# Kernel tuning notes

Measured on AMD Instinct MI355X. Metric: run time of the kernel, lower is better.

The kernel has to match this reference:

```python
import jax, jax.numpy as jnp
import numpy as np

# Representation: lvals=[0,1] -> nreps NL=2, dim DIM=1+3=4; mult=8; kqv conv out_mult=3*mult
N, K, EDGE_DIM, HID = 10000, 16, 32, 64
MULT, NL, DIM = 8, 2, 4
OUT_MULT = 3 * MULT
E = N * K
NHEADS = 4
HEAD_DIM = MULT * DIM // NHEADS  # 8


def setup_inputs() -> dict:
    key = jax.random.key(0)
    ks = jax.random.split(key, 9)
    out_flat = NL * NL * MULT * OUT_MULT  # 768
    return {
        "basis1": jax.random.normal(ks[0], (E, DIM, NL), jnp.float32),
        "basis2": jax.random.normal(ks[1], (E, NL, DIM), jnp.float32),
        "edge_feats": jax.random.normal(ks[2], (E, EDGE_DIM), jnp.float32),
        "f": jax.random.normal(ks[3], (N, MULT, DIM), jnp.float32),
        "W1": jax.random.normal(ks[4], (HID, EDGE_DIM), jnp.float32) / np.sqrt(EDGE_DIM).astype(np.float32),
        "b1": jnp.zeros((HID,), jnp.float32),
        "W2": jax.random.normal(ks[5], (out_flat, HID), jnp.float32) / np.sqrt(HID).astype(np.float32),
        "b2": jnp.zeros((out_flat,), jnp.float32),
        "neighbor_idx": jax.random.randint(ks[6], (N, K), 0, N, dtype=jnp.int32),
    }


def reference(basis1, basis2, edge_feats, f, W1, b1, W2, b2, neighbor_idx):
    src = neighbor_idx.reshape(-1)  # (E,) source node per edge
    # RadialWeight: 2-layer MLP edge_feats -> per-edge TP weights (E, NL*OUT_MULT, NL*MULT)
    h = jax.nn.relu(edge_feats @ W1.T + b1)
    rw = (h @ W2.T + b2).reshape(E, NL * OUT_MULT, NL * MULT)
    # EquivariantConvolution: gather + small batched matmuls
    f_src = f[src]  # (E, MULT, DIM)
    tmp = jnp.einsum('emd,edl->eml', f_src, basis1).reshape(E, NL * MULT, 1)
    tmp = (rw @ tmp).reshape(E, OUT_MULT, NL)
    kqv = jnp.einsum('eml,eld->emd', tmp, basis2)  # (E, 3*MULT, DIM)
    # split fused k/q/v along multiplicity (repr_h.rep2.mult = 3*mult)
    k_, q_, v_ = jnp.split(kqv.reshape(N, K, OUT_MULT, DIM), 3, axis=2)  # each (N,K,MULT,DIM)
    k_ = k_.reshape(N, K, NHEADS, HEAD_DIM)
    v_ = v_.reshape(N, K, NHEADS, HEAD_DIM)
    q_node = q_.reshape(N, K, NHEADS, HEAD_DIM).mean(axis=1)  # per-node query (N,H,hd)
    scale = HEAD_DIM ** -0.5
    scores = jnp.einsum('nhd,nkhd->nhk', q_node, k_) * scale  # (N,H,K)
    w = jax.nn.softmax(scores, axis=-1)
    out = jnp.einsum('nhk,nkhd->nhd', w, v_)  # (N,H,hd)
    return out.reshape(N, MULT, DIM)
```

## Files before the change

kernel.cpp:

```cpp
#include <hip/hip_runtime.h>
#include <hip/hip_bf16.h>
#include <math.h>

#define N_NODES 10000
#define KNBR    16
#define EDGEF   32
#define HID     64
#define MULT    8
#define NL      2
#define DIM     4
#define OUT_MULT 24
#define NHEADS  4
#define HEAD_DIM 8
#define E_TOT   (N_NODES*KNBR)

#define EPB 128
#define TPB 128
#define NTILE 4
#define NODES_PB 8
#define NSLICE 33

typedef float    f32x4 __attribute__((ext_vector_type(4)));
typedef _Float16 f16x8 __attribute__((ext_vector_type(8)));

#define BF1_HALVES (4*64*8)
#define BF2_HALVES (3*NSLICE*64*8)
#define WS_HALVES  (BF1_HALVES + BF2_HALVES)

__global__ __launch_bounds__(256)
void esa_prep(const float* __restrict__ W1, const float* __restrict__ W2,
              const float* __restrict__ b2, _Float16* __restrict__ wsh)
{
    int i = blockIdx.x * 256 + threadIdx.x;
    if (i >= WS_HALVES) return;
    float v;
    if (i < BF1_HALVES) {
        int j = i & 7, lane = (i >> 3) & 63, t = i >> 9;
        int k = ((lane >> 4) << 3) + j;
        int n = (t << 4) + (lane & 15);
        v = W1[n * EDGEF + k];
    } else {
        int i2 = i - BF1_HALVES;
        int j = i2 & 7, lane = (i2 >> 3) & 63;
        int st = i2 >> 9;
        int s = st % NSLICE, t = st / NSLICE;
        int k = (s << 5) + ((lane >> 4) << 3) + j;
        int n = (t << 4) + (lane & 15);
        if (k < 1024)      v = W2[(n * 16 + (k >> 6)) * HID + (k & 63)];
        else if (k < 1040) v = b2[n * 16 + (k - 1024)];
        else               v = 0.f;
    }
    wsh[i] = (_Float16)v;
}

__global__ __launch_bounds__(TPB, 2)
void esa_main(const float* __restrict__ basis1, const float* __restrict__ basis2,
              const float* __restrict__ edge_feats, const float* __restrict__ f,
              const float* __restrict__ b1, const int* __restrict__ nbr,
              const _Float16* __restrict__ wsh, float* __restrict__ out)
{
    __shared__ __align__(16) unsigned char smem[32768];
    _Float16* hls = (_Float16*)smem;
    _Float16* tpl = (_Float16*)(smem + 18432);
    float*    t2  = (float*)smem;
    float*    b2l = (float*)(smem + 26624);

    const int tid  = threadIdx.x;
    const int eb   = blockIdx.x * EPB;
    const int lane = tid & 63;
    const int w    = tid >> 6;
    const int lo   = lane & 15, hi = lane >> 4;

    {
        const int el = tid;
        const int e  = eb + el;
        const int src = nbr[e];
        const float4* b1p = (const float4*)(basis1 + (size_t)e * 8);
        float4 u0 = b1p[0], u1 = b1p[1];
        float bl0[4] = {u0.x, u0.z, u1.x, u1.z};
        float bl1[4] = {u0.y, u0.w, u1.y, u1.w};
        const float4* fp = (const float4*)(f + (size_t)src * 32);
        _Float16 tpv[16];
        #pragma unroll
        for (int m = 0; m < 8; ++m) {
            float4 fv = fp[m];
            float a0 = fv.x*bl0[0] + fv.y*bl0[1] + fv.z*bl0[2] + fv.w*bl0[3];
            float a1 = fv.x*bl1[0] + fv.y*bl1[1] + fv.z*bl1[2] + fv.w*bl1[3];
            tpv[m*2+0] = (_Float16)a0;
            tpv[m*2+1] = (_Float16)a1;
        }
        *(f16x8*)(tpl + el*16)     = *(f16x8*)&tpv[0];
        *(f16x8*)(tpl + el*16 + 8) = *(f16x8*)&tpv[8];
        const float4* b2p = (const float4*)(basis2 + (size_t)e * 8);
        *(float4*)(b2l + el*12)     = b2p[0];
        *(float4*)(b2l + el*12 + 4) = b2p[1];
    }

    {
        float b1v[4];
        #pragma unroll
        for (int t = 0; t < 4; ++t) b1v[t] = b1[t*16 + lo];
        f16x8 afr[NTILE];
        #pragma unroll
        for (int mt = 0; mt < NTILE; ++mt) {
            size_t eg = (size_t)(eb + w*64 + mt*16 + lo);
            const float4* p = (const float4*)(edge_feats + eg*32 + hi*8);
            float4 x0 = p[0], x1 = p[1];
            f16x8 a;
            a[0]=(_Float16)x0.x; a[1]=(_Float16)x0.y; a[2]=(_Float16)x0.z; a[3]=(_Float16)x0.w;
            a[4]=(_Float16)x1.x; a[5]=(_Float16)x1.y; a[6]=(_Float16)x1.z; a[7]=(_Float16)x1.w;
            afr[mt] = a;
        }
        #pragma unroll
        for (int t = 0; t < 4; ++t) {
            f16x8 bfr = *(const f16x8*)(wsh + ((size_t)(t*64 + lane)) * 8);
            #pragma unroll
            for (int mt = 0; mt < NTILE; ++mt) {
                f32x4 acc = {0.f, 0.f, 0.f, 0.f};
                acc = __builtin_amdgcn_mfma_f32_16x16x32_f16(afr[mt], bfr, acc, 0, 0, 0);
                #pragma unroll
                for (int r = 0; r < 4; ++r) {
                    float hv = acc[r] + b1v[t];
                    hv = hv > 0.f ? hv : 0.f;
                    int el = w*64 + mt*16 + hi*4 + r;
                    hls[el*72 + t*16 + lo] = (_Float16)hv;
                }
            }
        }
    }
    __syncthreads();

    f32x4 acc[NTILE][3];
    #pragma unroll
    for (int mt = 0; mt < NTILE; ++mt)
        #pragma unroll
        for (int t = 0; t < 3; ++t)
            acc[mt][t] = (f32x4){0.f, 0.f, 0.f, 0.f};

    {
        const _Float16* Bf2 = wsh + BF1_HALVES;
        const _Float16* hp[NTILE];
        f16x8 tpA[NTILE], tpB[NTILE];
        #pragma unroll
        for (int mt = 0; mt < NTILE; ++mt) {
            const int e_mt = w*64 + mt*16 + lo;
            hp[mt]  = hls + e_mt*72 + hi*8;
            tpA[mt] = *(const f16x8*)(tpl + e_mt*16);
            tpB[mt] = *(const f16x8*)(tpl + e_mt*16 + 8);
        }

        #pragma unroll
        for (int s = 0; s < 32; ++s) {
            const int c  = s >> 1;
            const int sh = s & 1;
            f16x8 bfr[3];
            #pragma unroll
            for (int t = 0; t < 3; ++t)
                bfr[t] = *(const f16x8*)(Bf2 + ((size_t)((t*NSLICE + s)*64 + lane)) * 8);
            #pragma unroll
            for (int mt = 0; mt < NTILE; ++mt) {
                _Float16 t0 = (c < 8) ? tpA[mt][c & 7] : tpB[mt][c & 7];
                f16x8 ts = {t0,t0,t0,t0,t0,t0,t0,t0};
                f16x8 h  = *(const f16x8*)(hp[mt] + sh*32);
                f16x8 a  = h * ts;
                #pragma unroll
                for (int t = 0; t < 3; ++t)
                    acc[mt][t] = __builtin_amdgcn_mfma_f32_16x16x32_f16(a, bfr[t], acc[mt][t], 0, 0, 0);
            }
        }
        {
            f16x8 z = {(_Float16)0,(_Float16)0,(_Float16)0,(_Float16)0,
                       (_Float16)0,(_Float16)0,(_Float16)0,(_Float16)0};
            f16x8 bfr[3];
            #pragma unroll
            for (int t = 0; t < 3; ++t)
                bfr[t] = *(const f16x8*)(Bf2 + ((size_t)((t*NSLICE + 32)*64 + lane)) * 8);
            #pragma unroll
            for (int mt = 0; mt < NTILE; ++mt) {
                f16x8 a = (hi == 0) ? tpA[mt] : (hi == 1) ? tpB[mt] : z;
                #pragma unroll
                for (int t = 0; t < 3; ++t)
                    acc[mt][t] = __builtin_amdgcn_mfma_f32_16x16x32_f16(a, bfr[t], acc[mt][t], 0, 0, 0);
            }
        }
    }

    __syncthreads();
    #pragma unroll
    for (int mt = 0; mt < NTILE; ++mt)
        #pragma unroll
        for (int t = 0; t < 3; ++t)
            #pragma unroll
            for (int r = 0; r < 4; ++r)
                t2[(w*64 + mt*16 + hi*4 + r)*52 + t*16 + lo] = acc[mt][t][r];
    __syncthreads();

    const int kk = lane >> 2, hh = lane & 3;
    #pragma unroll
    for (int it = 0; it < 4; ++it) {
        int nl = it*2 + w;
        int node = blockIdx.x * NODES_PB + nl;
        int el = nl*16 + kk;
        const float* trow = t2 + el*52;
        float4 tk = *(const float4*)(trow + hh*4);
        float4 tq = *(const float4*)(trow + 16 + hh*4);
        float4 tv = *(const float4*)(trow + 32 + hh*4);
        float4 bl0 = *(const float4*)(b2l + el*12);
        float4 bl1 = *(const float4*)(b2l + el*12 + 4);
        float k8[8], q8[8], v8[8];
        const float* B0 = (const float*)&bl0;
        const float* B1 = (const float*)&bl1;
        #pragma unroll
        for (int d = 0; d < 4; ++d) {
            k8[d]   = tk.x*B0[d] + tk.y*B1[d];
            k8[4+d] = tk.z*B0[d] + tk.w*B1[d];
            q8[d]   = tq.x*B0[d] + tq.y*B1[d];
            q8[4+d] = tq.z*B0[d] + tq.w*B1[d];
            v8[d]   = tv.x*B0[d] + tv.y*B1[d];
            v8[4+d] = tv.z*B0[d] + tv.w*B1[d];
        }
        float qn[8];
        #pragma unroll
        for (int i = 0; i < 8; ++i) qn[i] = q8[i];
        #pragma unroll
        for (int m = 4; m <= 32; m <<= 1)
            #pragma unroll
            for (int i = 0; i < 8; ++i) qn[i] += __shfl_xor(qn[i], m);
        float s = 0.f;
        #pragma unroll
        for (int i = 0; i < 8; ++i) s += qn[i]*k8[i];
        s *= 0.0220970869120796f;

        float mx = s;
        #pragma unroll
        for (int m = 4; m <= 32; m <<= 1) mx = fmaxf(mx, __shfl_xor(mx, m));
        float ex = __expf(s - mx);
        float den = ex;
        #pragma unroll
        for (int m = 4; m <= 32; m <<= 1) den += __shfl_xor(den, m);
        float wgt = ex / den;

        float o[8];
        #pragma unroll
        for (int i = 0; i < 8; ++i) o[i] = wgt * v8[i];
        #pragma unroll
        for (int m = 4; m <= 32; m <<= 1)
            #pragma unroll
            for (int i = 0; i < 8; ++i) o[i] += __shfl_xor(o[i], m);
        if (kk == 0) {
            float4* dst = (float4*)(out + (size_t)node*32 + hh*8);
            dst[0] = make_float4(o[0], o[1], o[2], o[3]);
            dst[1] = make_float4(o[4], o[5], o[6], o[7]);
        }
    }
}

extern "C" void kernel_launch(void* const* d_in, const int* in_sizes, int n_in,
                              void* d_out, int out_size, void* d_ws, size_t ws_size,
                              hipStream_t stream) {
    const float* basis1     = (const float*)d_in[0];
    const float* basis2     = (const float*)d_in[1];
    const float* edge_feats = (const float*)d_in[2];
    const float* f          = (const float*)d_in[3];
    const float* W1         = (const float*)d_in[4];
    const float* b1         = (const float*)d_in[5];
    const float* W2         = (const float*)d_in[6];
    const float* b2         = (const float*)d_in[7];
    const int*   nbr        = (const int*)d_in[8];
    float* out = (float*)d_out;
    _Float16* wsh = (_Float16*)d_ws;

    esa_prep<<<(WS_HALVES + 255)/256, 256, 0, stream>>>(W1, W2, b2, wsh);
    esa_main<<<E_TOT/EPB, TPB, 0, stream>>>(basis1, basis2, edge_feats, f,
                                            b1, nbr, wsh, out);
}
```

Before: 124.9 us.

## Double-buffer W2 fragments into LDS via async global_load_lds with larger blocks

Doubles the block to 256 threads and 256 edges (16 nodes). The second-layer weight fragments are now staged through a double-buffered LDS ring using async global-to-LDS loads, prefetched two chunks ahead, instead of being read from global memory inside the MFMA loop. The h operands are also hoisted into registers once. The aim is to overlap weight fetch latency with MFMA work and cut redundant global traffic. In exchange, LDS use rises to 80KB and a barrier is added per chunk, which may limit occupancy to one block per CU despite the launch bound of 2.

```diff
diff --git a/kernel.cpp b/kernel.cpp
--- a/kernel.cpp
+++ b/kernel.cpp
@@ -6,19 +6,15 @@
 #define KNBR    16
 #define EDGEF   32
 #define HID     64
-#define MULT    8
-#define NL      2
-#define DIM     4
-#define OUT_MULT 24
-#define NHEADS  4
-#define HEAD_DIM 8
 #define E_TOT   (N_NODES*KNBR)
 
-#define EPB 128
-#define TPB 128
+#define EPB 256
+#define TPB 256
 #define NTILE 4
-#define NODES_PB 8
+#define NODES_PB 16
 #define NSLICE 33
+#define CHUNK 4
+#define NCHUNK 8
 
 typedef float    f32x4 __attribute__((ext_vector_type(4)));
 typedef _Float16 f16x8 __attribute__((ext_vector_type(8)));
@@ -53,23 +49,39 @@
     wsh[i] = (_Float16)v;
 }
 
+__device__ __forceinline__ void issue16(const _Float16* g, unsigned char* l) {
+    __builtin_amdgcn_global_load_lds(
+        (const __attribute__((address_space(1))) void*)g,
+        (__attribute__((address_space(3))) void*)(void*)l, 16, 0, 0);
+}
+
 __global__ __launch_bounds__(TPB, 2)
 void esa_main(const float* __restrict__ basis1, const float* __restrict__ basis2,
               const float* __restrict__ edge_feats, const float* __restrict__ f,
               const float* __restrict__ b1, const int* __restrict__ nbr,
               const _Float16* __restrict__ wsh, float* __restrict__ out)
 {
-    __shared__ __align__(16) unsigned char smem[32768];
-    _Float16* hls = (_Float16*)smem;
-    _Float16* tpl = (_Float16*)(smem + 18432);
+    __shared__ __align__(16) unsigned char smem[81920];
+    _Float16* hls = (_Float16*)(smem + 24576);
+    _Float16* tpl = (_Float16*)(smem + 61440);
+    float*    b2l = (float*)(smem + 69632);
     float*    t2  = (float*)smem;
-    float*    b2l = (float*)(smem + 26624);
 
     const int tid  = threadIdx.x;
     const int eb   = blockIdx.x * EPB;
     const int lane = tid & 63;
     const int w    = tid >> 6;
     const int lo   = lane & 15, hi = lane >> 4;
+
+    const _Float16* Bf2 = wsh + BF1_HALVES;
+
+    #pragma unroll
+    for (int j = 0; j < 3; ++j) {
+        issue16(Bf2 + ((size_t)((j*NSLICE + (0*CHUNK + w))*64) + lane)*8,
+                smem + 0*12288 + (w*3 + j)*1024);
+        issue16(Bf2 + ((size_t)((j*NSLICE + (1*CHUNK + w))*64) + lane)*8,
+                smem + 1*12288 + (w*3 + j)*1024);
+    }
 
     {
         const int el = tid;
@@ -137,55 +149,63 @@
         for (int t = 0; t < 3; ++t)
             acc[mt][t] = (f32x4){0.f, 0.f, 0.f, 0.f};
 
-    {
-        const _Float16* Bf2 = wsh + BF1_HALVES;
-        const _Float16* hp[NTILE];
-        f16x8 tpA[NTILE], tpB[NTILE];
-        #pragma unroll
-        for (int mt = 0; mt < NTILE; ++mt) {
-            const int e_mt = w*64 + mt*16 + lo;
-            hp[mt]  = hls + e_mt*72 + hi*8;
-            tpA[mt] = *(const f16x8*)(tpl + e_mt*16);
-            tpB[mt] = *(const f16x8*)(tpl + e_mt*16 + 8);
-        }
-
-        #pragma unroll
-        for (int s = 0; s < 32; ++s) {
-            const int c  = s >> 1;
+    f16x8 tpA[NTILE], tpB[NTILE], hA[NTILE], hB[NTILE];
+    #pragma unroll
+    for (int mt = 0; mt < NTILE; ++mt) {
+        const int e_mt = w*64 + mt*16 + lo;
+        tpA[mt] = *(const f16x8*)(tpl + e_mt*16);
+        tpB[mt] = *(const f16x8*)(tpl + e_mt*16 + 8);
+        hA[mt]  = *(const f16x8*)(hls + e_mt*72 + hi*8);
+        hB[mt]  = *(const f16x8*)(hls + e_mt*72 + 32 + hi*8);
+    }
+
+    #pragma unroll
+    for (int c = 0; c < NCHUNK; ++c) {
+        const _Float16* buf = (const _Float16*)(smem + (c & 1)*12288);
+        #pragma unroll
+        for (int sc = 0; sc < CHUNK; ++sc) {
+            const int s  = c*CHUNK + sc;
+            const int cc = s >> 1;
             const int sh = s & 1;
             f16x8 bfr[3];
             #pragma unroll
             for (int t = 0; t < 3; ++t)
-                bfr[t] = *(const f16x8*)(Bf2 + ((size_t)((t*NSLICE + s)*64 + lane)) * 8);
+                bfr[t] = *(const f16x8*)(buf + ((sc*3 + t)*64 + lane)*8);
             #pragma unroll
             for (int mt = 0; mt < NTILE; ++mt) {
-                _Float16 t0 = (c < 8) ? tpA[mt][c & 7] : tpB[mt][c & 7];
-                f16x8 ts = {t0,t0,t0,t0,t0,t0,t0,t0};
-                f16x8 h  = *(const f16x8*)(hp[mt] + sh*32);
-                f16x8 a  = h * ts;
+                _Float16 s0 = (cc < 8) ? tpA[mt][cc & 7] : tpB[mt][cc & 7];
+                f16x8 a = (sh ? hB[mt] : hA[mt]) * (f16x8){s0,s0,s0,s0,s0,s0,s0,s0};
                 #pragma unroll
                 for (int t = 0; t < 3; ++t)
                     acc[mt][t] = __builtin_amdgcn_mfma_f32_16x16x32_f16(a, bfr[t], acc[mt][t], 0, 0, 0);
             }
         }
-        {
-            f16x8 z = {(_Float16)0,(_Float16)0,(_Float16)0,(_Float16)0,
-                       (_Float16)0,(_Float16)0,(_Float16)0,(_Float16)0};
-            f16x8 bfr[3];
+        __syncthreads();
+        if (c + 2 < NCHUNK) {
+            const int s = (c + 2)*CHUNK + w;
+            #pragma unroll
+            for (int j = 0; j < 3; ++j)
+                issue16(Bf2 + ((size_t)((j*NSLICE + s)*64) + lane)*8,
+                        smem + (c & 1)*12288 + (w*3 + j)*1024);
+        }
+    }
+
+    {
+        f16x8 z = {(_Float16)0,(_Float16)0,(_Float16)0,(_Float16)0,
+                   (_Float16)0,(_Float16)0,(_Float16)0,(_Float16)0};
+        f16x8 bfr[3];
+        #pragma unroll
+        for (int t = 0; t < 3; ++t)
+            bfr[t] = *(const f16x8*)(Bf2 + ((size_t)((t*NSLICE + 32)*64 + lane)) * 8);
+        #pragma unroll
+        for (int mt = 0; mt < NTILE; ++mt) {
+            f16x8 a = (hi == 0) ? tpA[mt] : (hi == 1) ? tpB[mt] : z;
             #pragma unroll
             for (int t = 0; t < 3; ++t)
-                bfr[t] = *(const f16x8*)(Bf2 + ((size_t)((t*NSLICE + 32)*64 + lane)) * 8);
-            #pragma unroll
-            for (int mt = 0; mt < NTILE; ++mt) {
-                f16x8 a = (hi == 0) ? tpA[mt] : (hi == 1) ? tpB[mt] : z;
-                #pragma unroll
-                for (int t = 0; t < 3; ++t)
-                    acc[mt][t] = __builtin_amdgcn_mfma_f32_16x16x32_f16(a, bfr[t], acc[mt][t], 0, 0, 0);
-            }
-        }
-    }
-
-    __syncthreads();
+                acc[mt][t] = __builtin_amdgcn_mfma_f32_16x16x32_f16(a, bfr[t], acc[mt][t], 0, 0, 0);
+        }
+    }
+
     #pragma unroll
     for (int mt = 0; mt < NTILE; ++mt)
         #pragma unroll
@@ -198,7 +218,7 @@
     const int kk = lane >> 2, hh = lane & 3;
     #pragma unroll
     for (int it = 0; it < 4; ++it) {
-        int nl = it*2 + w;
+        int nl = it*4 + w;
         int node = blockIdx.x * NODES_PB + nl;
         int el = nl*16 + kk;
         const float* trow = t2 + el*52;
```

Result: faster. 118.0 us (-5.5%).
